# Kernel tuning notes

Hardware: AMD Instinct MI355X
Metric: run time of the kernel (lower is better)

## Reference

```python
import jax, jax.numpy as jnp
import numpy as np

B, S, DIM = 8, 1, 2048
H = 16
QLR, KVLR = 1536, 512
DN, DR, DV = 128, 64, 128      # qk_nope, qk_rope, v head dims
START = 8191                    # start_pos; end_pos = START + S = 8192
EPS = 1e-6
SCALE = (DN + DR) ** -0.5


def _rms(x, w):
    # F.rms_norm: x / sqrt(mean(x^2)+eps) * w
    return x * w * jax.lax.rsqrt(jnp.mean(jnp.square(x), axis=-1, keepdims=True) + EPS)


def _rope(x, cos, sin):
    # x: [..., r]; consecutive pairs (x0,x1) treated as complex, multiplied by cos+i*sin
    xr, xi = x[..., 0::2], x[..., 1::2]
    out_r = xr * cos - xi * sin
    out_i = xr * sin + xi * cos
    return jnp.stack([out_r, out_i], axis=-1).reshape(x.shape)


def setup_inputs() -> dict:
    key = jax.random.key(0)
    ks = jax.random.split(key, 12)
    # rotary tables for the single decode position
    inv_freq = 1.0 / (10000.0 ** (np.arange(0, DR, 2, dtype=np.float32) / DR))  # [DR/2]
    pos = np.arange(START, START + S, dtype=np.float32)[:, None]                # [S,1]
    ang = pos * inv_freq[None, :]                                               # [S, DR/2]
    return {
        "x": jax.random.normal(ks[0], (B, S, DIM), jnp.float32),
        "start_pos": START,
        "freqs_cos": jnp.asarray(np.cos(ang)),
        "freqs_sin": jnp.asarray(np.sin(ang)),
        "kv_cache_prefix": jax.random.normal(ks[1], (B, START, KVLR), jnp.float32),
        "pe_cache_prefix": jax.random.normal(ks[2], (B, START, DR), jnp.float32),
        "wq_a_w": jax.random.normal(ks[3], (QLR, DIM), jnp.float32) * 0.02,
        "wq_a_b": jnp.zeros((QLR,), jnp.float32),
        "q_norm_w": jnp.ones((QLR,), jnp.float32),
        "wq_b_w": jax.random.normal(ks[4], (H * (DN + DR), QLR), jnp.float32) * 0.02,
        "wq_b_b": jnp.zeros((H * (DN + DR),), jnp.float32),
        "wkv_a_w": jax.random.normal(ks[5], (KVLR + DR, DIM), jnp.float32) * 0.02,
        "wkv_a_b": jnp.zeros((KVLR + DR,), jnp.float32),
        "kv_norm_w": jnp.ones((KVLR,), jnp.float32),
        "wkv_b_w": jax.random.normal(ks[6], (H * (DN + DV), KVLR), jnp.float32) * 0.02,
        "wo_w": jax.random.normal(ks[7], (DIM, H * DV), jnp.float32) * 0.02,
        "wo_b": jnp.zeros((DIM,), jnp.float32),
    }


def reference(x, start_pos, freqs_cos, freqs_sin, kv_cache_prefix, pe_cache_prefix,
              wq_a_w, wq_a_b, q_norm_w, wq_b_w, wq_b_b,
              wkv_a_w, wkv_a_b, kv_norm_w, wkv_b_w, wo_w, wo_b):
    b, s, _ = x.shape
    # low-rank query projection
    q = _rms(x @ wq_a_w.T + wq_a_b, q_norm_w) @ wq_b_w.T + wq_b_b
    q = q.reshape(b, s, H, DN + DR)
    q_nope, q_pe = q[..., :DN], q[..., DN:]
    cos = freqs_cos[None, :, None, :]  # [1,s,1,DR/2]
    sin = freqs_sin[None, :, None, :]
    q_pe = _rope(q_pe, cos, sin)
    # compressed KV + rope key branch
    kvpe = x @ wkv_a_w.T + wkv_a_b               # [b,s,KVLR+DR]
    kv, k_pe = kvpe[..., :KVLR], kvpe[..., KVLR:]
    k_pe = _rope(k_pe[:, :, None, :], cos, sin)[:, :, 0, :]
    # weight absorption: project q_nope into latent space through wkv_b's K-part
    wkv_b = wkv_b_w.reshape(H, DN + DV, KVLR)
    q_abs = jnp.einsum('bshd,hdc->bshc', q_nope, wkv_b[:, :DN])
    # append current step to caches
    kv_cache = jnp.concatenate([kv_cache_prefix, _rms(kv, kv_norm_w)], axis=1)  # [b,t,KVLR]
    pe_cache = jnp.concatenate([pe_cache_prefix, k_pe], axis=1)                 # [b,t,DR]
    # attention in latent space (seqlen=1 decode -> no causal mask needed)
    scores = (jnp.einsum('bshc,btc->bsht', q_abs, kv_cache)
              + jnp.einsum('bshr,btr->bsht', q_pe, pe_cache)) * SCALE
    attn = jax.nn.softmax(scores.astype(jnp.float32), axis=-1).astype(x.dtype)
    out = jnp.einsum('bsht,btc->bshc', attn, kv_cache)
    out = jnp.einsum('bshc,hdc->bshd', out, wkv_b[:, DN:])  # V-part of wkv_b
    return out.reshape(b, s, H * DV) @ wo_w.T + wo_b
```

## Files before the change

### kernel.cpp

```cpp
#include <hip/hip_runtime.h>
#include <math.h>

namespace {
constexpr int B_   = 8;
constexpr int DIM_ = 2048;
constexpr int H_   = 16;
constexpr int QLR_ = 1536;
constexpr int KVLR_= 512;
constexpr int DN_  = 128;
constexpr int DR_  = 64;
constexpr int DV_  = 128;
constexpr int TPRE_= 8191;
constexpr int CE_  = 576;
constexpr int NCH_ = 32;
constexpr int CT_  = 256;
constexpr int TS_  = 16;
constexpr int PSTR_= 20;
constexpr float EPS_ = 1e-6f;
constexpr float SCALE_ = 0.07216878364870322f;

constexpr size_t WS_QLAT  = 0;
constexpr size_t WS_KVPE  = WS_QLAT  + (size_t)B_*QLR_;
constexpr size_t WS_KVNEW = WS_KVPE  + (size_t)B_*CE_;
constexpr size_t WS_PENEW = WS_KVNEW + (size_t)B_*KVLR_;
constexpr size_t WS_QRS   = WS_PENEW + (size_t)B_*DR_;
constexpr size_t WS_QNOPE = WS_QRS   + (size_t)B_;
constexpr size_t WS_QT    = WS_QNOPE + (size_t)B_*H_*DN_;
constexpr size_t WS_MLOC  = WS_QT    + (size_t)B_*CE_*H_;
constexpr size_t WS_LLOC  = WS_MLOC  + (size_t)B_*H_*NCH_;
constexpr size_t WS_OUT2  = WS_LLOC  + (size_t)B_*H_*NCH_;
constexpr size_t WS_OPART = WS_OUT2  + (size_t)B_*DIM_;
}

__device__ __forceinline__ void gload16(const float* src, float* ldsDst) {
  __builtin_amdgcn_global_load_lds((const __attribute__((address_space(1))) void*)src,
                                   (__attribute__((address_space(3))) void*)ldsDst,
                                   16, 0, 0);
}

__global__ __launch_bounds__(256) void mla_k1(const float* __restrict__ x,
                                              const float* __restrict__ wqa,
                                              const float* __restrict__ bqa,
                                              const float* __restrict__ wkva,
                                              const float* __restrict__ bkva,
                                              float* __restrict__ ws) {
  const int w = threadIdx.x >> 6, l = threadIdx.x & 63;
  const int r = blockIdx.x * 4 + w;
  const float* W; const float* bias; float* out; int rr; int ostride;
  if (r < QLR_) { W = wqa;  bias = bqa;  out = ws + WS_QLAT; rr = r;        ostride = QLR_; }
  else          { W = wkva; bias = bkva; out = ws + WS_KVPE; rr = r - QLR_; ostride = CE_;  }
  const float4* wp = (const float4*)(W + (size_t)rr * DIM_);
  const float4* x4 = (const float4*)x;
  float4 wv[8];
#pragma unroll
  for (int j = 0; j < 8; ++j) wv[j] = wp[l + 64 * j];
  float acc[B_];
#pragma unroll
  for (int b = 0; b < B_; ++b) acc[b] = 0.f;
#pragma unroll
  for (int b = 0; b < B_; ++b) {
#pragma unroll
    for (int j = 0; j < 8; ++j) {
      const float4 xv = x4[b * (DIM_ / 4) + l + 64 * j];
      acc[b] = fmaf(wv[j].x, xv.x, fmaf(wv[j].y, xv.y, fmaf(wv[j].z, xv.z, fmaf(wv[j].w, xv.w, acc[b]))));
    }
  }
#pragma unroll
  for (int b = 0; b < B_; ++b)
#pragma unroll
    for (int s = 32; s; s >>= 1) acc[b] += __shfl_xor(acc[b], s);
  if (l == 0) {
    const float b0 = bias[rr];
#pragma unroll
    for (int b = 0; b < B_; ++b) out[b * ostride + rr] = acc[b] + b0;
  }
}

__global__ __launch_bounds__(256) void mla_k2(const float* __restrict__ kvnw,
                                              const float* __restrict__ fcos,
                                              const float* __restrict__ fsin,
                                              float* __restrict__ ws) {
  const int tid = threadIdx.x;
  const int b = tid >> 5, i = tid & 31;
  const float* kvpe = ws + WS_KVPE + b * CE_;
  float ss = 0.f;
#pragma unroll
  for (int j = 0; j < KVLR_ / 32; ++j) { const float v = kvpe[i + 32 * j]; ss = fmaf(v, v, ss); }
#pragma unroll
  for (int s = 16; s; s >>= 1) ss += __shfl_xor(ss, s, 32);
  const float scale = 1.0f / sqrtf(ss / (float)KVLR_ + EPS_);
  float* kvn = ws + WS_KVNEW + b * KVLR_;
#pragma unroll
  for (int j = 0; j < KVLR_ / 32; ++j) {
    const int c = i + 32 * j;
    kvn[c] = kvpe[c] * kvnw[c] * scale;
  }
  {
    const float xr = kvpe[KVLR_ + 2 * i], xi = kvpe[KVLR_ + 2 * i + 1];
    const float c = fcos[i], s = fsin[i];
    float* pen = ws + WS_PENEW + b * DR_;
    pen[2 * i]     = xr * c - xi * s;
    pen[2 * i + 1] = xr * s + xi * c;
  }
  {
    const float* p = ws + WS_QLAT + b * QLR_;
    float sq = 0.f;
#pragma unroll
    for (int j = 0; j < QLR_ / 32; ++j) { const float v = p[i + 32 * j]; sq = fmaf(v, v, sq); }
#pragma unroll
    for (int s = 16; s; s >>= 1) sq += __shfl_xor(sq, s, 32);
    if (i == 0) ws[WS_QRS + b] = 1.0f / sqrtf(sq / (float)QLR_ + EPS_);
  }
}

__global__ __launch_bounds__(256) void mla_k3(const float* __restrict__ qnw,
                                              const float* __restrict__ wqb,
                                              const float* __restrict__ bqb,
                                              const float* __restrict__ fcos,
                                              const float* __restrict__ fsin,
                                              float* __restrict__ ws) {
  const int w = threadIdx.x >> 6, l = threadIdx.x & 63;
  const int r0 = blockIdx.x * 8 + w * 2;
  const float4* w0p = (const float4*)(wqb + (size_t)r0 * QLR_);
  const float4* w1p = (const float4*)(wqb + (size_t)(r0 + 1) * QLR_);
  const float4* g4  = (const float4*)qnw;
  const float4* x4  = (const float4*)(ws + WS_QLAT);
  float4 wg0[6], wg1[6];
#pragma unroll
  for (int j = 0; j < 6; ++j) {
    const int c4 = l + 64 * j;
    const float4 a = w0p[c4], bb = w1p[c4], g = g4[c4];
    wg0[j].x = a.x * g.x; wg0[j].y = a.y * g.y; wg0[j].z = a.z * g.z; wg0[j].w = a.w * g.w;
    wg1[j].x = bb.x * g.x; wg1[j].y = bb.y * g.y; wg1[j].z = bb.z * g.z; wg1[j].w = bb.w * g.w;
  }
  float acc0[B_], acc1[B_];
#pragma unroll
  for (int b = 0; b < B_; ++b) { acc0[b] = 0.f; acc1[b] = 0.f; }
#pragma unroll
  for (int b = 0; b < B_; ++b) {
#pragma unroll
    for (int j = 0; j < 6; ++j) {
      const float4 xv = x4[b * (QLR_ / 4) + l + 64 * j];
      acc0[b] = fmaf(wg0[j].x, xv.x, fmaf(wg0[j].y, xv.y, fmaf(wg0[j].z, xv.z, fmaf(wg0[j].w, xv.w, acc0[b]))));
      acc1[b] = fmaf(wg1[j].x, xv.x, fmaf(wg1[j].y, xv.y, fmaf(wg1[j].z, xv.z, fmaf(wg1[j].w, xv.w, acc1[b]))));
    }
  }
#pragma unroll
  for (int b = 0; b < B_; ++b)
#pragma unroll
    for (int s = 32; s; s >>= 1) {
      acc0[b] += __shfl_xor(acc0[b], s);
      acc1[b] += __shfl_xor(acc1[b], s);
    }
  if (l == 0) {
    const int h = r0 / (DN_ + DR_);
    const int j0 = r0 - h * (DN_ + DR_);
    const float b0 = bqb[r0], b1 = bqb[r0 + 1];
    if (j0 < DN_) {
      float* qn = ws + WS_QNOPE;
#pragma unroll
      for (int b = 0; b < B_; ++b) {
        const float sb = ws[WS_QRS + b];
        qn[(b * H_ + h) * DN_ + j0]     = acc0[b] * sb + b0;
        qn[(b * H_ + h) * DN_ + j0 + 1] = acc1[b] * sb + b1;
      }
    } else {
      const int i = (j0 - DN_) >> 1;
      const float c = fcos[i], s = fsin[i];
      float* qT = ws + WS_QT;
#pragma unroll
      for (int b = 0; b < B_; ++b) {
        const float sb = ws[WS_QRS + b];
        const float xr = acc0[b] * sb + b0, xi = acc1[b] * sb + b1;
        qT[((size_t)b * CE_ + KVLR_ + 2 * i) * H_ + h]     = xr * c - xi * s;
        qT[((size_t)b * CE_ + KVLR_ + 2 * i + 1) * H_ + h] = xr * s + xi * c;
      }
    }
  }
}

__global__ __launch_bounds__(256) void mla_k4(const float* __restrict__ wkvb,
                                              float* __restrict__ ws) {
  __shared__ float red[7 * 32 * B_];
  const int h = blockIdx.y;
  const int strip = blockIdx.x;
  const int tid = threadIdx.x;
  const int c = tid & 31, dg = tid >> 5;
  const int cg = strip * 32 + c;
  const float* qn = ws + WS_QNOPE;
  float acc[B_];
#pragma unroll
  for (int b = 0; b < B_; ++b) acc[b] = 0.f;
  const float* wp = wkvb + (size_t)h * 256 * KVLR_ + cg;
#pragma unroll
  for (int dd = 0; dd < 16; ++dd) {
    const int d = dg * 16 + dd;
    const float wv = wp[(size_t)d * KVLR_];
#pragma unroll
    for (int b = 0; b < B_; ++b) acc[b] = fmaf(qn[(b * H_ + h) * DN_ + d], wv, acc[b]);
  }
  if (dg > 0) {
#pragma unroll
    for (int b = 0; b < B_; ++b) red[(((dg - 1) * 32) + c) * B_ + b] = acc[b];
  }
  __syncthreads();
  if (dg == 0) {
    float* qT = ws + WS_QT;
#pragma unroll
    for (int b = 0; b < B_; ++b) {
      float v = acc[b];
#pragma unroll
      for (int g = 0; g < 7; ++g) v += red[(g * 32 + c) * B_ + b];
      qT[((size_t)b * CE_ + cg) * H_ + h] = v;
    }
  }
}

__global__ __launch_bounds__(512, 2) void mla_k5(const float* __restrict__ kvpre,
                                                 const float* __restrict__ pepre,
                                                 float* __restrict__ ws) {
  __shared__ float kv_lds[2][TS_ * CE_];
  __shared__ float q_lds[9248];
  __shared__ float p_lds[TS_ * PSTR_];
  __shared__ float m_st[H_], l_st[H_], f_st[H_];

  const int b = blockIdx.y;
  const int chunk = blockIdx.x;
  const int t0 = chunk * CT_;
  const int tid = threadIdx.x;
  const int w = tid >> 6, l = tid & 63;
  const float* kvnew = ws + WS_KVNEW + b * KVLR_;
  const float* penew = ws + WS_PENEW + b * DR_;

  auto stageKV = [&](float* buf, int s) {
    const int ts0 = t0 + s * TS_;
    for (int i = w; i < (TS_ * CE_) / 256; i += 8) {
      const int f = i * 64 + l;
      const int tl = f / 144;
      const int c4 = f - tl * 144;
      const int tg = ts0 + tl;
      const float* src;
      if (tg < TPRE_) {
        src = (c4 < 128) ? (kvpre + ((size_t)b * TPRE_ + tg) * KVLR_ + 4 * c4)
                         : (pepre + ((size_t)b * TPRE_ + tg) * DR_ + 4 * (c4 - 128));
      } else {
        src = (c4 < 128) ? (kvnew + 4 * c4) : (penew + 4 * (c4 - 128));
      }
      gload16(src, buf + (size_t)i * 256);
    }
  };

  stageKV(kv_lds[0], 0);

  {
    const float4* qsrc = (const float4*)(ws + WS_QT + (size_t)b * CE_ * H_);
#pragma unroll
    for (int k = 0; k < 5; ++k) {
      const int idx = tid + 512 * k;
      if (idx < (CE_ * H_) / 4) {
        const float4 v = qsrc[idx];
        const int c = idx >> 2, hq = idx & 3;
        *(float4*)(q_lds + c * 16 + hq * 4 + 4 * (c / 72)) = v;
      }
    }
    if (tid < H_) { m_st[tid] = -3.4e38f; l_st[tid] = 0.f; }
  }

  const int c8 = l >> 3;
  const int rlo = l & 7;
  const int t2 = ((w & 3) << 1) + (rlo >> 2);
  const int h4 = rlo & 3;
  const int c4p = tid >> 2, h4p = tid & 3;

  float o[4][4];
#pragma unroll
  for (int cc = 0; cc < 4; ++cc)
#pragma unroll
    for (int hh = 0; hh < 4; ++hh) o[cc][hh] = 0.f;

  for (int s = 0; s < CT_ / TS_; ++s) {
    __syncthreads();
    if (s + 1 < CT_ / TS_) stageKV(kv_lds[(s + 1) & 1], s + 1);
    const float* bufc = kv_lds[s & 1];

    if (tid < 256) {
      const float* r0 = bufc + (2 * t2) * CE_ + c8 * 72;
      const float* r1 = r0 + CE_;
      const float* qb = q_lds + (c8 * 72) * 16 + 4 * c8 + 4 * h4;
      float acc0[4] = {0.f, 0.f, 0.f, 0.f};
      float acc1[4] = {0.f, 0.f, 0.f, 0.f};
#pragma unroll
      for (int j = 0; j < 18; ++j) {
        const float4 k0 = *(const float4*)(r0 + 4 * j);
        const float4 k1 = *(const float4*)(r1 + 4 * j);
        const float4 q0 = *(const float4*)(qb + (4 * j + 0) * 16);
        const float4 q1 = *(const float4*)(qb + (4 * j + 1) * 16);
        const float4 q2 = *(const float4*)(qb + (4 * j + 2) * 16);
        const float4 q3 = *(const float4*)(qb + (4 * j + 3) * 16);
        acc0[0] = fmaf(k0.x, q0.x, fmaf(k0.y, q1.x, fmaf(k0.z, q2.x, fmaf(k0.w, q3.x, acc0[0]))));
        acc0[1] = fmaf(k0.x, q0.y, fmaf(k0.y, q1.y, fmaf(k0.z, q2.y, fmaf(k0.w, q3.y, acc0[1]))));
        acc0[2] = fmaf(k0.x, q0.z, fmaf(k0.y, q1.z, fmaf(k0.z, q2.z, fmaf(k0.w, q3.z, acc0[2]))));
        acc0[3] = fmaf(k0.x, q0.w, fmaf(k0.y, q1.w, fmaf(k0.z, q2.w, fmaf(k0.w, q3.w, acc0[3]))));
        acc1[0] = fmaf(k1.x, q0.x, fmaf(k1.y, q1.x, fmaf(k1.z, q2.x, fmaf(k1.w, q3.x, acc1[0]))));
        acc1[1] = fmaf(k1.x, q0.y, fmaf(k1.y, q1.y, fmaf(k1.z, q2.y, fmaf(k1.w, q3.y, acc1[1]))));
        acc1[2] = fmaf(k1.x, q0.z, fmaf(k1.y, q1.z, fmaf(k1.z, q2.z, fmaf(k1.w, q3.z, acc1[2]))));
        acc1[3] = fmaf(k1.x, q0.w, fmaf(k1.y, q1.w, fmaf(k1.z, q2.w, fmaf(k1.w, q3.w, acc1[3]))));
      }
#pragma unroll
      for (int d = 8; d <= 32; d <<= 1) {
#pragma unroll
        for (int hh = 0; hh < 4; ++hh) {
          acc0[hh] += __shfl_xor(acc0[hh], d);
          acc1[hh] += __shfl_xor(acc1[hh], d);
        }
      }
      if (c8 == 0) {
        float4 v0, v1;
        v0.x = acc0[0] * SCALE_; v0.y = acc0[1] * SCALE_;
        v0.z = acc0[2] * SCALE_; v0.w = acc0[3] * SCALE_;
        v1.x = acc1[0] * SCALE_; v1.y = acc1[1] * SCALE_;
        v1.z = acc1[2] * SCALE_; v1.w = acc1[3] * SCALE_;
        *(float4*)(p_lds + (2 * t2) * PSTR_ + 4 * h4)     = v0;
        *(float4*)(p_lds + (2 * t2 + 1) * PSTR_ + 4 * h4) = v1;
      }
    }
    __syncthreads();

    if (tid < 256) {
      const int h2 = tid >> 4, tg = tid & 15;
      const float sv = p_lds[tg * PSTR_ + h2];
      float msub = sv;
#pragma unroll
      for (int d = 1; d < 16; d <<= 1) msub = fmaxf(msub, __shfl_xor(msub, d, 16));
      const float mold = m_st[h2];
      const float mnew = fmaxf(mold, msub);
      const float e = __expf(sv - mnew);
      float lsum = e;
#pragma unroll
      for (int d = 1; d < 16; d <<= 1) lsum += __shfl_xor(lsum, d, 16);
      p_lds[tg * PSTR_ + h2] = e;
      if (tg == 0) {
        const float fac = __expf(mold - mnew);
        f_st[h2] = fac;
        l_st[h2] = l_st[h2] * fac + lsum;
        m_st[h2] = mnew;
      }
    }
    __syncthreads();

    {
      const float4 fv = *(const float4*)(f_st + 4 * h4p);
#pragma unroll
      for (int cc = 0; cc < 4; ++cc) {
        o[cc][0] *= fv.x; o[cc][1] *= fv.y; o[cc][2] *= fv.z; o[cc][3] *= fv.w;
      }
#pragma unroll
      for (int t = 0; t < TS_; ++t) {
        const float4 kq = *(const float4*)(bufc + t * CE_ + 4 * c4p);
        const float4 pq = *(const float4*)(p_lds + t * PSTR_ + 4 * h4p);
        o[0][0] = fmaf(pq.x, kq.x, o[0][0]); o[0][1] = fmaf(pq.y, kq.x, o[0][1]);
        o[0][2] = fmaf(pq.z, kq.x, o[0][2]); o[0][3] = fmaf(pq.w, kq.x, o[0][3]);
        o[1][0] = fmaf(pq.x, kq.y, o[1][0]); o[1][1] = fmaf(pq.y, kq.y, o[1][1]);
        o[1][2] = fmaf(pq.z, kq.y, o[1][2]); o[1][3] = fmaf(pq.w, kq.y, o[1][3]);
        o[2][0] = fmaf(pq.x, kq.z, o[2][0]); o[2][1] = fmaf(pq.y, kq.z, o[2][1]);
        o[2][2] = fmaf(pq.z, kq.z, o[2][2]); o[2][3] = fmaf(pq.w, kq.z, o[2][3]);
        o[3][0] = fmaf(pq.x, kq.w, o[3][0]); o[3][1] = fmaf(pq.y, kq.w, o[3][1]);
        o[3][2] = fmaf(pq.z, kq.w, o[3][2]); o[3][3] = fmaf(pq.w, kq.w, o[3][3]);
      }
    }
  }

  {
    float* Op = ws + WS_OPART;
#pragma unroll
    for (int hh = 0; hh < 4; ++hh) {
      const int h = 4 * h4p + hh;
      float4 v;
      v.x = o[0][hh]; v.y = o[1][hh]; v.z = o[2][hh]; v.w = o[3][hh];
      *(float4*)(Op + ((size_t)(b * H_ + h) * NCH_ + chunk) * KVLR_ + 4 * c4p) = v;
    }
    if (tid < H_) {
      ws[WS_MLOC + (b * H_ + tid) * NCH_ + chunk] = m_st[tid];
      ws[WS_LLOC + (b * H_ + tid) * NCH_ + chunk] = l_st[tid];
    }
  }
}

__global__ __launch_bounds__(256) void mla_k6(const float* __restrict__ wkvb,
                                              float* __restrict__ ws) {
  const int h = blockIdx.x, b = blockIdx.y;
  __shared__ float wgt[NCH_];
  __shared__ float ao[KVLR_];
  __shared__ float Linv;
  const int tid = threadIdx.x;
  if (tid < NCH_) {
    const float m = ws[WS_MLOC + (b * H_ + h) * NCH_ + tid];
    float M = m;
#pragma unroll
    for (int s = 16; s; s >>= 1) M = fmaxf(M, __shfl_xor(M, s, 32));
    const float wv = __expf(m - M);
    wgt[tid] = wv;
    float lv = ws[WS_LLOC + (b * H_ + h) * NCH_ + tid] * wv;
#pragma unroll
    for (int s = 16; s; s >>= 1) lv += __shfl_xor(lv, s, 32);
    if (tid == 0) Linv = 1.0f / lv;
  }
  __syncthreads();
  const float* Ob = ws + WS_OPART + (size_t)(b * H_ + h) * NCH_ * KVLR_;
  float s0 = 0.f, s1 = 0.f;
#pragma unroll 4
  for (int i = 0; i < NCH_; ++i) {
    const float wv = wgt[i];
    s0 = fmaf(wv, Ob[(size_t)i * KVLR_ + tid], s0);
    s1 = fmaf(wv, Ob[(size_t)i * KVLR_ + tid + 256], s1);
  }
  const float li = Linv;
  ao[tid] = s0 * li;
  ao[tid + 256] = s1 * li;
  __syncthreads();
  const int v = tid >> 1, half = tid & 1;
  const float* w2 = wkvb + ((size_t)h * 256 + DN_ + v) * KVLR_ + half * 256;
  const float* a = ao + half * 256;
  float s = 0.f;
#pragma unroll
  for (int c = 0; c < 256; c += 4) {
    const float4 wv = *(const float4*)(w2 + c);
    s = fmaf(wv.x, a[c], s);
    s = fmaf(wv.y, a[c + 1], s);
    s = fmaf(wv.z, a[c + 2], s);
    s = fmaf(wv.w, a[c + 3], s);
  }
  s += __shfl_xor(s, 1);
  if (half == 0) ws[WS_OUT2 + b * DIM_ + h * DV_ + v] = s;
}

__global__ __launch_bounds__(256) void mla_k7(const float* __restrict__ wo,
                                              const float* __restrict__ wob,
                                              const float* __restrict__ ws,
                                              float* __restrict__ out) {
  const int w = threadIdx.x >> 6, l = threadIdx.x & 63;
  const int r = blockIdx.x * 4 + w;
  const float4* wp = (const float4*)(wo + (size_t)r * DIM_);
  const float4* x4 = (const float4*)(ws + WS_OUT2);
  float4 wv[8];
#pragma unroll
  for (int j = 0; j < 8; ++j) wv[j] = wp[l + 64 * j];
  float acc[B_];
#pragma unroll
  for (int b = 0; b < B_; ++b) acc[b] = 0.f;
#pragma unroll
  for (int b = 0; b < B_; ++b) {
#pragma unroll
    for (int j = 0; j < 8; ++j) {
      const float4 xv = x4[b * (DIM_ / 4) + l + 64 * j];
      acc[b] = fmaf(wv[j].x, xv.x, fmaf(wv[j].y, xv.y, fmaf(wv[j].z, xv.z, fmaf(wv[j].w, xv.w, acc[b]))));
    }
  }
#pragma unroll
  for (int b = 0; b < B_; ++b)
#pragma unroll
    for (int s = 32; s; s >>= 1) acc[b] += __shfl_xor(acc[b], s);
  if (l == 0) {
    const float b0 = wob[r];
#pragma unroll
    for (int b = 0; b < B_; ++b) out[b * DIM_ + r] = acc[b] + b0;
  }
}

extern "C" void kernel_launch(void* const* d_in, const int* in_sizes, int n_in,
                              void* d_out, int out_size, void* d_ws, size_t ws_size,
                              hipStream_t stream) {
  (void)in_sizes; (void)n_in; (void)out_size; (void)ws_size;
  const float* x     = (const float*)d_in[0];
  const float* fcos  = (const float*)d_in[2];
  const float* fsin  = (const float*)d_in[3];
  const float* kvpre = (const float*)d_in[4];
  const float* pepre = (const float*)d_in[5];
  const float* wqa   = (const float*)d_in[6];
  const float* bqa   = (const float*)d_in[7];
  const float* qnw   = (const float*)d_in[8];
  const float* wqb   = (const float*)d_in[9];
  const float* bqb   = (const float*)d_in[10];
  const float* wkva  = (const float*)d_in[11];
  const float* bkva  = (const float*)d_in[12];
  const float* kvnw  = (const float*)d_in[13];
  const float* wkvb  = (const float*)d_in[14];
  const float* wo    = (const float*)d_in[15];
  const float* wob   = (const float*)d_in[16];
  float* ws  = (float*)d_ws;
  float* out = (float*)d_out;

  mla_k1<<<dim3((QLR_ + CE_) / 4), dim3(256), 0, stream>>>(x, wqa, bqa, wkva, bkva, ws);
  mla_k2<<<dim3(1), dim3(256), 0, stream>>>(kvnw, fcos, fsin, ws);
  mla_k3<<<dim3(H_ * (DN_ + DR_) / 8), dim3(256), 0, stream>>>(qnw, wqb, bqb, fcos, fsin, ws);
  mla_k4<<<dim3(16, H_), dim3(256), 0, stream>>>(wkvb, ws);
  mla_k5<<<dim3(NCH_, B_), dim3(512), 0, stream>>>(kvpre, pepre, ws);
  mla_k6<<<dim3(H_, B_), dim3(256), 0, stream>>>(wkvb, ws);
  mla_k7<<<dim3(DIM_ / 4), dim3(256), 0, stream>>>(wo, wob, ws, out);
}
```

Baseline: 366.6 us.

## Keep query in registers, double KV tile size, use DPP reductions in MLA attention

The query latent layout is changed to head-major so each thread of the attention kernel holds two heads' 36-element query slices in registers, replacing the LDS-staged query. The KV tile grows from 16 to 32 tokens, so the score phase uses all 512 threads with each thread covering 8 tokens, and the 16-lane partial sums are reduced with DPP row operations. This removes query LDS traffic and halves the number of barrier-separated tile iterations. In exchange it raises register pressure (72 floats of query plus accumulators) and doubles LDS for the KV buffers, which may limit occupancy at the requested 2 blocks per CU.

```diff
diff --git a/kernel.cpp b/kernel.cpp
--- a/kernel.cpp
+++ b/kernel.cpp
@@ -14,7 +14,7 @@
 constexpr int CE_  = 576;
 constexpr int NCH_ = 32;
 constexpr int CT_  = 256;
-constexpr int TS_  = 16;
+constexpr int TS_  = 32;
 constexpr int PSTR_= 20;
 constexpr float EPS_ = 1e-6f;
 constexpr float SCALE_ = 0.07216878364870322f;
@@ -36,6 +36,18 @@
   __builtin_amdgcn_global_load_lds((const __attribute__((address_space(1))) void*)src,
                                    (__attribute__((address_space(3))) void*)ldsDst,
                                    16, 0, 0);
+}
+
+__device__ __forceinline__ float rsum16(float v) {
+  int x = __float_as_int(v);
+  v += __int_as_float(__builtin_amdgcn_update_dpp(0, x, 0xB1, 0xF, 0xF, true));
+  x = __float_as_int(v);
+  v += __int_as_float(__builtin_amdgcn_update_dpp(0, x, 0x4E, 0xF, 0xF, true));
+  x = __float_as_int(v);
+  v += __int_as_float(__builtin_amdgcn_update_dpp(0, x, 0x141, 0xF, 0xF, true));
+  x = __float_as_int(v);
+  v += __int_as_float(__builtin_amdgcn_update_dpp(0, x, 0x140, 0xF, 0xF, true));
+  return v;
 }
 
 __global__ __launch_bounds__(256) void mla_k1(const float* __restrict__ x,
@@ -167,13 +179,13 @@
     } else {
       const int i = (j0 - DN_) >> 1;
       const float c = fcos[i], s = fsin[i];
-      float* qT = ws + WS_QT;
+      float* qTT = ws + WS_QT;
 #pragma unroll
       for (int b = 0; b < B_; ++b) {
         const float sb = ws[WS_QRS + b];
         const float xr = acc0[b] * sb + b0, xi = acc1[b] * sb + b1;
-        qT[((size_t)b * CE_ + KVLR_ + 2 * i) * H_ + h]     = xr * c - xi * s;
-        qT[((size_t)b * CE_ + KVLR_ + 2 * i + 1) * H_ + h] = xr * s + xi * c;
+        qTT[((size_t)(b * H_ + h)) * CE_ + KVLR_ + 2 * i]     = xr * c - xi * s;
+        qTT[((size_t)(b * H_ + h)) * CE_ + KVLR_ + 2 * i + 1] = xr * s + xi * c;
       }
     }
   }
@@ -205,13 +217,13 @@
   }
   __syncthreads();
   if (dg == 0) {
-    float* qT = ws + WS_QT;
+    float* qTT = ws + WS_QT;
 #pragma unroll
     for (int b = 0; b < B_; ++b) {
       float v = acc[b];
 #pragma unroll
       for (int g = 0; g < 7; ++g) v += red[(g * 32 + c) * B_ + b];
-      qT[((size_t)b * CE_ + cg) * H_ + h] = v;
+      qTT[((size_t)(b * H_ + h)) * CE_ + cg] = v;
     }
   }
 }
@@ -220,57 +232,55 @@
                                                  const float* __restrict__ pepre,
                                                  float* __restrict__ ws) {
   __shared__ float kv_lds[2][TS_ * CE_];
-  __shared__ float q_lds[9248];
   __shared__ float p_lds[TS_ * PSTR_];
   __shared__ float m_st[H_], l_st[H_], f_st[H_];
 
-  const int b = blockIdx.y;
-  const int chunk = blockIdx.x;
+  const int b = blockIdx.y, chunk = blockIdx.x;
   const int t0 = chunk * CT_;
   const int tid = threadIdx.x;
   const int w = tid >> 6, l = tid & 63;
+  const int cs = l & 15;
+  const int hl = l >> 4;
+  const int tg = w >> 1;
+  const int hg = (w & 1) * 4 + hl;
+  const int c4p = tid >> 2, h4p = tid & 3;
+
   const float* kvnew = ws + WS_KVNEW + b * KVLR_;
   const float* penew = ws + WS_PENEW + b * DR_;
 
   auto stageKV = [&](float* buf, int s) {
     const int ts0 = t0 + s * TS_;
-    for (int i = w; i < (TS_ * CE_) / 256; i += 8) {
+#pragma unroll
+    for (int k = 0; k < 9; ++k) {
+      const int i = w + 8 * k;
       const int f = i * 64 + l;
       const int tl = f / 144;
       const int c4 = f - tl * 144;
-      const int tg = ts0 + tl;
+      const int tgl = ts0 + tl;
       const float* src;
-      if (tg < TPRE_) {
-        src = (c4 < 128) ? (kvpre + ((size_t)b * TPRE_ + tg) * KVLR_ + 4 * c4)
-                         : (pepre + ((size_t)b * TPRE_ + tg) * DR_ + 4 * (c4 - 128));
+      if (tgl < TPRE_) {
+        src = (c4 < 128) ? (kvpre + ((size_t)b * TPRE_ + tgl) * KVLR_ + 4 * c4)
+                         : (pepre + ((size_t)b * TPRE_ + tgl) * DR_ + 4 * (c4 - 128));
       } else {
         src = (c4 < 128) ? (kvnew + 4 * c4) : (penew + 4 * (c4 - 128));
       }
-      gload16(src, buf + (size_t)i * 256);
+      gload16(src, buf + (size_t)i * 64 * 4);
     }
   };
 
   stageKV(kv_lds[0], 0);
 
+  float4 q0v[9], q1v[9];
   {
-    const float4* qsrc = (const float4*)(ws + WS_QT + (size_t)b * CE_ * H_);
-#pragma unroll
-    for (int k = 0; k < 5; ++k) {
-      const int idx = tid + 512 * k;
-      if (idx < (CE_ * H_) / 4) {
-        const float4 v = qsrc[idx];
-        const int c = idx >> 2, hq = idx & 3;
-        *(float4*)(q_lds + c * 16 + hq * 4 + 4 * (c / 72)) = v;
-      }
-    }
-    if (tid < H_) { m_st[tid] = -3.4e38f; l_st[tid] = 0.f; }
-  }
-
-  const int c8 = l >> 3;
-  const int rlo = l & 7;
-  const int t2 = ((w & 3) << 1) + (rlo >> 2);
-  const int h4 = rlo & 3;
-  const int c4p = tid >> 2, h4p = tid & 3;
+    const float* qb0 = ws + WS_QT + ((size_t)(b * H_) + 2 * hg) * CE_ + cs * 36;
+    const float* qb1 = qb0 + CE_;
+#pragma unroll
+    for (int j = 0; j < 9; ++j) {
+      q0v[j] = *(const float4*)(qb0 + 4 * j);
+      q1v[j] = *(const float4*)(qb1 + 4 * j);
+    }
+  }
+  if (tid < H_) { m_st[tid] = -3.4e38f; l_st[tid] = 0.f; }
 
   float o[4][4];
 #pragma unroll
@@ -283,63 +293,53 @@
     if (s + 1 < CT_ / TS_) stageKV(kv_lds[(s + 1) & 1], s + 1);
     const float* bufc = kv_lds[s & 1];
 
-    if (tid < 256) {
-      const float* r0 = bufc + (2 * t2) * CE_ + c8 * 72;
-      const float* r1 = r0 + CE_;
-      const float* qb = q_lds + (c8 * 72) * 16 + 4 * c8 + 4 * h4;
-      float acc0[4] = {0.f, 0.f, 0.f, 0.f};
-      float acc1[4] = {0.f, 0.f, 0.f, 0.f};
-#pragma unroll
-      for (int j = 0; j < 18; ++j) {
-        const float4 k0 = *(const float4*)(r0 + 4 * j);
-        const float4 k1 = *(const float4*)(r1 + 4 * j);
-        const float4 q0 = *(const float4*)(qb + (4 * j + 0) * 16);
-        const float4 q1 = *(const float4*)(qb + (4 * j + 1) * 16);
-        const float4 q2 = *(const float4*)(qb + (4 * j + 2) * 16);
-        const float4 q3 = *(const float4*)(qb + (4 * j + 3) * 16);
-        acc0[0] = fmaf(k0.x, q0.x, fmaf(k0.y, q1.x, fmaf(k0.z, q2.x, fmaf(k0.w, q3.x, acc0[0]))));
-        acc0[1] = fmaf(k0.x, q0.y, fmaf(k0.y, q1.y, fmaf(k0.z, q2.y, fmaf(k0.w, q3.y, acc0[1]))));
-        acc0[2] = fmaf(k0.x, q0.z, fmaf(k0.y, q1.z, fmaf(k0.z, q2.z, fmaf(k0.w, q3.z, acc0[2]))));
-        acc0[3] = fmaf(k0.x, q0.w, fmaf(k0.y, q1.w, fmaf(k0.z, q2.w, fmaf(k0.w, q3.w, acc0[3]))));
-        acc1[0] = fmaf(k1.x, q0.x, fmaf(k1.y, q1.x, fmaf(k1.z, q2.x, fmaf(k1.w, q3.x, acc1[0]))));
-        acc1[1] = fmaf(k1.x, q0.y, fmaf(k1.y, q1.y, fmaf(k1.z, q2.y, fmaf(k1.w, q3.y, acc1[1]))));
-        acc1[2] = fmaf(k1.x, q0.z, fmaf(k1.y, q1.z, fmaf(k1.z, q2.z, fmaf(k1.w, q3.z, acc1[2]))));
-        acc1[3] = fmaf(k1.x, q0.w, fmaf(k1.y, q1.w, fmaf(k1.z, q2.w, fmaf(k1.w, q3.w, acc1[3]))));
-      }
-#pragma unroll
-      for (int d = 8; d <= 32; d <<= 1) {
-#pragma unroll
-        for (int hh = 0; hh < 4; ++hh) {
-          acc0[hh] += __shfl_xor(acc0[hh], d);
-          acc1[hh] += __shfl_xor(acc1[hh], d);
+    {
+      float acc[8][2];
+#pragma unroll
+      for (int tt = 0; tt < 8; ++tt) { acc[tt][0] = 0.f; acc[tt][1] = 0.f; }
+      const float* kb = bufc + (tg * 8) * CE_ + cs * 36;
+#pragma unroll
+      for (int j = 0; j < 9; ++j) {
+        float4 kv[8];
+#pragma unroll
+        for (int tt = 0; tt < 8; ++tt) kv[tt] = *(const float4*)(kb + tt * CE_ + 4 * j);
+#pragma unroll
+        for (int tt = 0; tt < 8; ++tt) {
+          const float4 k = kv[tt];
+          const float4 a = q0v[j], c = q1v[j];
+          acc[tt][0] = fmaf(k.x, a.x, fmaf(k.y, a.y, fmaf(k.z, a.z, fmaf(k.w, a.w, acc[tt][0]))));
+          acc[tt][1] = fmaf(k.x, c.x, fmaf(k.y, c.y, fmaf(k.z, c.z, fmaf(k.w, c.w, acc[tt][1]))));
         }
       }
-      if (c8 == 0) {
-        float4 v0, v1;
-        v0.x = acc0[0] * SCALE_; v0.y = acc0[1] * SCALE_;
-        v0.z = acc0[2] * SCALE_; v0.w = acc0[3] * SCALE_;
-        v1.x = acc1[0] * SCALE_; v1.y = acc1[1] * SCALE_;
-        v1.z = acc1[2] * SCALE_; v1.w = acc1[3] * SCALE_;
-        *(float4*)(p_lds + (2 * t2) * PSTR_ + 4 * h4)     = v0;
-        *(float4*)(p_lds + (2 * t2 + 1) * PSTR_ + 4 * h4) = v1;
+#pragma unroll
+      for (int tt = 0; tt < 8; ++tt) {
+        acc[tt][0] = rsum16(acc[tt][0]);
+        acc[tt][1] = rsum16(acc[tt][1]);
+      }
+      if (cs == 0) {
+#pragma unroll
+        for (int tt = 0; tt < 8; ++tt) {
+          float2 v; v.x = acc[tt][0] * SCALE_; v.y = acc[tt][1] * SCALE_;
+          *(float2*)(p_lds + (tg * 8 + tt) * PSTR_ + 2 * hg) = v;
+        }
       }
     }
     __syncthreads();
 
-    if (tid < 256) {
-      const int h2 = tid >> 4, tg = tid & 15;
-      const float sv = p_lds[tg * PSTR_ + h2];
+    {
+      const int h2 = tid >> 5, tl2 = tid & 31;
+      const float sv = p_lds[tl2 * PSTR_ + h2];
       float msub = sv;
 #pragma unroll
-      for (int d = 1; d < 16; d <<= 1) msub = fmaxf(msub, __shfl_xor(msub, d, 16));
+      for (int d = 16; d; d >>= 1) msub = fmaxf(msub, __shfl_xor(msub, d, 32));
       const float mold = m_st[h2];
       const float mnew = fmaxf(mold, msub);
       const float e = __expf(sv - mnew);
       float lsum = e;
 #pragma unroll
-      for (int d = 1; d < 16; d <<= 1) lsum += __shfl_xor(lsum, d, 16);
-      p_lds[tg * PSTR_ + h2] = e;
-      if (tg == 0) {
+      for (int d = 16; d; d >>= 1) lsum += __shfl_xor(lsum, d, 32);
+      p_lds[tl2 * PSTR_ + h2] = e;
+      if (tl2 == 0) {
         const float fac = __expf(mold - mnew);
         f_st[h2] = fac;
         l_st[h2] = l_st[h2] * fac + lsum;
@@ -354,7 +354,7 @@
       for (int cc = 0; cc < 4; ++cc) {
         o[cc][0] *= fv.x; o[cc][1] *= fv.y; o[cc][2] *= fv.z; o[cc][3] *= fv.w;
       }
-#pragma unroll
+#pragma unroll 8
       for (int t = 0; t < TS_; ++t) {
         const float4 kq = *(const float4*)(bufc + t * CE_ + 4 * c4p);
         const float4 pq = *(const float4*)(p_lds + t * PSTR_ + 4 * h4p);
```

After: 421.7 us. 15.0% more time.
